# Kernel optimization log

Hardware: AMD Instinct MI355X
Metric: run time of the kernel (lower is better)

## Reference

```python
import jax, jax.numpy as jnp
import numpy as np

FEAT_STRIDE = 32  # 520 // 16
POOL = 7          # adaptive_avg_pool2d target (7,7)
C = 8             # channels consumed as (2 classes x 4 coords)


def setup_inputs() -> dict:
    key = jax.random.key(0)
    k1, k2, k3 = jax.random.split(key, 3)
    H = W = 1024
    conv_out = jax.random.normal(k1, (1, C, H, W), dtype=jnp.float32)
    n = 8192
    # sample pixel-space coords in [0, H*FEAT_STRIDE) and sort so min<=max per axis
    ys = jnp.sort(jax.random.randint(k2, (n, 2), 0, H * FEAT_STRIDE), axis=1)
    xs = jnp.sort(jax.random.randint(k3, (n, 2), 0, W * FEAT_STRIDE), axis=1)
    rois = jnp.stack([ys[:, 0], xs[:, 0], ys[:, 1], xs[:, 1]], axis=1).astype(jnp.int64)
    return {"conv_out": conv_out, "rois": rois}


def _adaptive_bounds(start, length):
    # PyTorch adaptive_avg_pool2d bin edges over [start, start+length)
    j = jnp.arange(POOL)
    lo = start + (j * length) // POOL
    hi = start + ((j + 1) * length + POOL - 1) // POOL  # ceil div
    return lo, hi


def _forward(conv_out, rois):
    r = rois // FEAT_STRIDE
    x = conv_out[0]  # [C, H, W]
    # summed-area table, padded so sat[:, y, x] = sum over [0:y, 0:x)
    sat = jnp.pad(jnp.cumsum(jnp.cumsum(x, axis=1), axis=2),
                  ((0, 0), (1, 0), (1, 0)))  # [C, H+1, W+1]

    def pool_one(roi):
        ymin, xmin = roi[0], roi[1]
        ymax, xmax = roi[2] + 1, roi[3] + 1  # exclusive ends
        ylo, yhi = _adaptive_bounds(ymin, ymax - ymin)
        xlo, xhi = _adaptive_bounds(xmin, xmax - xmin)
        # 7x7 bin sums via inclusion-exclusion on SAT -> [C,7,7]
        s = (sat[:, yhi[:, None], xhi[None, :]]
             - sat[:, ylo[:, None], xhi[None, :]]
             - sat[:, yhi[:, None], xlo[None, :]]
             + sat[:, ylo[:, None], xlo[None, :]])
        area = ((yhi - ylo)[:, None] * (xhi - xlo)[None, :]).astype(s.dtype)
        block7 = s / area                       # adaptive_avg_pool2d -> (7,7)
        return block7.mean(axis=(1, 2))         # adaptive_avg_pool2d -> (1,1), [C]

    pooled = jax.vmap(pool_one)(r)              # [n, C]
    return pooled.reshape(-1, 2, 4)


def reference(conv_out, rois):
    return _forward(conv_out, rois)
```

## Files before the change

kernel.cpp:

```cpp
#include <hip/hip_runtime.h>
#include <cstddef>
#include <cstdint>

#define SATW 1025
#define W8   8200
#define NCH  8

__global__ __launch_bounds__(256) void rowscan_kernel(const float* __restrict__ in,
                                                      float* __restrict__ sat) {
    const int y    = blockIdx.x;
    const int t    = threadIdx.x;
    const int lane = t & 63;
    const int wv   = t >> 6;

    __shared__ float lds[NCH][1024];

    for (int k = 0; k < 2; ++k) {
        const int c = wv * 2 + k;
        const float4* r4 = (const float4*)(in + ((size_t)c * 1024 + y) * 1024);
        double chunkbase = 0.0;
#pragma unroll
        for (int j = 0; j < 4; ++j) {
            float4 a = r4[lane + 64 * j];
            double v0 = a.x, v1 = a.y, v2 = a.z, v3 = a.w;
            double s = v0 + v1 + v2 + v3;
            double ps = s;
#pragma unroll
            for (int off = 1; off < 64; off <<= 1) {
                double n = __shfl_up(ps, off, 64);
                if (lane >= off) ps += n;
            }
            double base = chunkbase + ps - s;
            double p0 = base + v0, p1 = p0 + v1, p2 = p1 + v2, p3 = p2 + v3;
            float4 o = make_float4((float)p0, (float)p1, (float)p2, (float)p3);
            ((float4*)lds[c])[lane + 64 * j] = o;
            chunkbase += __shfl(ps, 63, 64);
        }
    }
    __syncthreads();

    float* orow = sat + (size_t)(y + 1) * W8;
    for (int f4 = t; f4 < W8 / 4; f4 += 256) {
        int f = f4 * 4;
        float4 o;
        float* po = (float*)&o;
#pragma unroll
        for (int j = 0; j < 4; ++j) {
            int ff = f + j;
            int x = ff >> 3, c = ff & 7;
            po[j] = x ? lds[c][x - 1] : 0.0f;
        }
        ((float4*)orow)[f4] = o;
    }
}

__global__ void colsum_kernel(const float* __restrict__ sat,
                              double* __restrict__ partial, int R) {
    int f  = blockIdx.x * 256 + threadIdx.x;
    int ch = blockIdx.y;
    if (f >= W8) return;
    const float* p = sat + ((size_t)(1 + ch * R)) * W8 + f;
    double s = 0.0;
#pragma unroll 4
    for (int i = 0; i < R; ++i) s += (double)p[(size_t)i * W8];
    partial[(size_t)ch * W8 + f] = s;
}

__global__ void scanpartial_kernel(double* __restrict__ partial, int C) {
    int f = blockIdx.x * 256 + threadIdx.x;
    if (f >= W8) return;
    double run = 0.0;
    for (int ch = 0; ch < C; ++ch) {
        double v = partial[(size_t)ch * W8 + f];
        partial[(size_t)ch * W8 + f] = run;
        run += v;
    }
}

__global__ void colscan_kernel(float* __restrict__ sat,
                               const double* __restrict__ partial, int R) {
    int f  = blockIdx.x * 256 + threadIdx.x;
    int ch = blockIdx.y;
    if (f >= W8) return;
    double run = partial[(size_t)ch * W8 + f];
    if (ch == 0) sat[f] = 0.0f;
    float* p = sat + ((size_t)(1 + ch * R)) * W8 + f;
#pragma unroll 4
    for (int i = 0; i < R; ++i) {
        run += (double)p[(size_t)i * W8];
        p[(size_t)i * W8] = (float)run;
    }
}

__global__ __launch_bounds__(256) void pool_kernel(const float* __restrict__ sat,
                                                   const int* __restrict__ rois,
                                                   float* __restrict__ out,
                                                   int n_roi) {
    int lane = threadIdx.x & 63;
    int roi  = (blockIdx.x * blockDim.x + threadIdx.x) >> 6;
    if (roi >= n_roi) return;

    const int4 rv = ((const int4*)rois)[roi];
    int ymin = rv.x >> 5;
    int xmin = rv.y >> 5;
    int Ly   = (rv.z >> 5) + 1 - ymin;
    int Lx   = (rv.w >> 5) + 1 - xmin;

    double acc[NCH];
#pragma unroll
    for (int c = 0; c < NCH; ++c) acc[c] = 0.0;

    if (lane < 49) {
        int by = lane / 7;
        int bx = lane - by * 7;
        int ylo = ymin + (by * Ly) / 7;
        int yhi = ymin + ((by + 1) * Ly + 6) / 7;
        int xlo = xmin + (bx * Lx) / 7;
        int xhi = xmin + ((bx + 1) * Lx + 6) / 7;
        double inv = 1.0 / (double)((yhi - ylo) * (xhi - xlo));

        const float4* hh = (const float4*)(sat + ((size_t)yhi * SATW + xhi) * NCH);
        const float4* lh = (const float4*)(sat + ((size_t)ylo * SATW + xhi) * NCH);
        const float4* hl = (const float4*)(sat + ((size_t)yhi * SATW + xlo) * NCH);
        const float4* ll = (const float4*)(sat + ((size_t)ylo * SATW + xlo) * NCH);
        float4 a0 = hh[0], a1 = hh[1];
        float4 b0 = lh[0], b1 = lh[1];
        float4 c0 = hl[0], c1 = hl[1];
        float4 d0 = ll[0], d1 = ll[1];
        const float* pa = (const float*)&a0;
        const float* pb = (const float*)&b0;
        const float* pc = (const float*)&c0;
        const float* pd = (const float*)&d0;
        float4 tmpa[2] = {a0, a1}, tmpb[2] = {b0, b1}, tmpc[2] = {c0, c1}, tmpd[2] = {d0, d1};
        const float* fa = (const float*)tmpa;
        const float* fb = (const float*)tmpb;
        const float* fc = (const float*)tmpc;
        const float* fd = (const float*)tmpd;
        (void)pa; (void)pb; (void)pc; (void)pd;
#pragma unroll
        for (int c = 0; c < NCH; ++c) {
            double v = (double)fa[c] - (double)fb[c] - (double)fc[c] + (double)fd[c];
            acc[c] = v * inv;
        }
    }

#pragma unroll
    for (int off = 32; off; off >>= 1) {
#pragma unroll
        for (int c = 0; c < NCH; ++c) acc[c] += __shfl_down(acc[c], off, 64);
    }

    if (lane == 0) {
        float4 o0 = make_float4((float)(acc[0] * (1.0 / 49.0)),
                                (float)(acc[1] * (1.0 / 49.0)),
                                (float)(acc[2] * (1.0 / 49.0)),
                                (float)(acc[3] * (1.0 / 49.0)));
        float4 o1 = make_float4((float)(acc[4] * (1.0 / 49.0)),
                                (float)(acc[5] * (1.0 / 49.0)),
                                (float)(acc[6] * (1.0 / 49.0)),
                                (float)(acc[7] * (1.0 / 49.0)));
        float4* po = (float4*)(out + (size_t)roi * NCH);
        po[0] = o0;
        po[1] = o1;
    }
}

extern "C" void kernel_launch(void* const* d_in, const int* in_sizes, int n_in,
                              void* d_out, int out_size, void* d_ws, size_t ws_size,
                              hipStream_t stream) {
    const float* conv = (const float*)d_in[0];
    const int*   rois = (const int*)d_in[1];
    float*       out  = (float*)d_out;
    int n_roi = in_sizes[1] / 4;

    const size_t sat_bytes = (size_t)SATW * W8 * 4;
    int C = 64;
    while (C > 8 && sat_bytes + (size_t)C * W8 * 8 > ws_size) C >>= 1;
    int R = 1024 / C;

    float*  sat     = (float*)d_ws;
    double* partial = (double*)((char*)d_ws + sat_bytes);

    rowscan_kernel<<<1024, 256, 0, stream>>>(conv, sat);
    colsum_kernel<<<dim3(33, C), 256, 0, stream>>>(sat, partial, R);
    scanpartial_kernel<<<33, 256, 0, stream>>>(partial, C);
    colscan_kernel<<<dim3(33, C), 256, 0, stream>>>(sat, partial, R);
    pool_kernel<<<(n_roi + 3) / 4, 256, 0, stream>>>(sat, rois, out, n_roi);
}
```

Before: 134.7 us.

## Replace three-pass column scan with single-pass decoupled look-back chained scan

The colsum, scanpartial and colscan kernels are replaced by one chained kernel. Each block takes a 16-row chunk of a 1024-wide column slice through a ticket counter, keeps the chunk in registers, publishes its aggregate, and looks back over earlier chunks' flags to get its prefix before writing the scanned rows. This removes one full read pass over the SAT and two kernel launches, in exchange for spin-waiting on flags and atomics. The control flags are zeroed inside the row-scan kernel.

```diff
diff --git a/kernel.cpp b/kernel.cpp
--- a/kernel.cpp
+++ b/kernel.cpp
@@ -5,13 +5,29 @@
 #define SATW 1025
 #define W8   8200
 #define NCH  8
+#define ROWS 16
+#define NCHUNK 64
+#define NSLICE 9
+#define SLICEW 1024
+
+#define SAT_BYTES ((size_t)SATW * W8 * 4)
+#define CTRL_OFF  ((SAT_BYTES + 255) & ~(size_t)255)
+#define CTRL_INTS (16 + NSLICE * NCHUNK)
+#define AGG_OFF   (CTRL_OFF + 4096)
+#define AGG_BYTES ((size_t)NSLICE * NCHUNK * SLICEW * 8)
+#define INCL_OFF  (AGG_OFF + AGG_BYTES)
 
 __global__ __launch_bounds__(256) void rowscan_kernel(const float* __restrict__ in,
-                                                      float* __restrict__ sat) {
+                                                      float* __restrict__ sat,
+                                                      int* __restrict__ ctrl) {
     const int y    = blockIdx.x;
     const int t    = threadIdx.x;
     const int lane = t & 63;
     const int wv   = t >> 6;
+
+    if (y == 0) {
+        for (int i = t; i < CTRL_INTS; i += 256) ctrl[i] = 0;
+    }
 
     __shared__ float lds[NCH][1024];
 
@@ -32,8 +48,8 @@
             }
             double base = chunkbase + ps - s;
             double p0 = base + v0, p1 = p0 + v1, p2 = p1 + v2, p3 = p2 + v3;
-            float4 o = make_float4((float)p0, (float)p1, (float)p2, (float)p3);
-            ((float4*)lds[c])[lane + 64 * j] = o;
+            ((float4*)lds[c])[lane + 64 * j] =
+                make_float4((float)p0, (float)p1, (float)p2, (float)p3);
             chunkbase += __shfl(ps, 63, 64);
         }
     }
@@ -54,41 +70,94 @@
     }
 }
 
-__global__ void colsum_kernel(const float* __restrict__ sat,
-                              double* __restrict__ partial, int R) {
-    int f  = blockIdx.x * 256 + threadIdx.x;
-    int ch = blockIdx.y;
-    if (f >= W8) return;
-    const float* p = sat + ((size_t)(1 + ch * R)) * W8 + f;
-    double s = 0.0;
-#pragma unroll 4
-    for (int i = 0; i < R; ++i) s += (double)p[(size_t)i * W8];
-    partial[(size_t)ch * W8 + f] = s;
-}
-
-__global__ void scanpartial_kernel(double* __restrict__ partial, int C) {
-    int f = blockIdx.x * 256 + threadIdx.x;
-    if (f >= W8) return;
-    double run = 0.0;
-    for (int ch = 0; ch < C; ++ch) {
-        double v = partial[(size_t)ch * W8 + f];
-        partial[(size_t)ch * W8 + f] = run;
-        run += v;
-    }
-}
-
-__global__ void colscan_kernel(float* __restrict__ sat,
-                               const double* __restrict__ partial, int R) {
-    int f  = blockIdx.x * 256 + threadIdx.x;
-    int ch = blockIdx.y;
-    if (f >= W8) return;
-    double run = partial[(size_t)ch * W8 + f];
-    if (ch == 0) sat[f] = 0.0f;
-    float* p = sat + ((size_t)(1 + ch * R)) * W8 + f;
-#pragma unroll 4
-    for (int i = 0; i < R; ++i) {
-        run += (double)p[(size_t)i * W8];
-        p[(size_t)i * W8] = (float)run;
+__global__ __launch_bounds__(256) void colscan_chained(float* __restrict__ sat,
+                                                       double* __restrict__ agg,
+                                                       double* __restrict__ incl,
+                                                       int* __restrict__ ctrl) {
+    const int slice = blockIdx.x;
+    const int t     = threadIdx.x;
+    int* tickets = ctrl;
+    int* flags   = ctrl + 16;
+
+    __shared__ int sh_chunk;
+    if (t == 0) sh_chunk = atomicAdd(&tickets[slice], 1);
+    __syncthreads();
+    const int chunk = sh_chunk;
+
+    const int  col = slice * SLICEW + t * 4;
+    const bool act = col < W8;
+
+    float4 r[ROWS];
+    double s0 = 0, s1 = 0, s2 = 0, s3 = 0;
+    float* base = sat + (size_t)(1 + chunk * ROWS) * W8 + col;
+    if (act) {
+#pragma unroll
+        for (int i = 0; i < ROWS; ++i) {
+            r[i] = *(const float4*)(base + (size_t)i * W8);
+            s0 += r[i].x; s1 += r[i].y; s2 += r[i].z; s3 += r[i].w;
+        }
+    }
+
+    const size_t vo  = ((size_t)slice * NCHUNK + chunk) * SLICEW + (size_t)t * 4;
+    int*         flg = &flags[slice * NCHUNK + chunk];
+    double e0 = 0, e1 = 0, e2 = 0, e3 = 0;
+
+    if (chunk == 0) {
+        __hip_atomic_store(&incl[vo + 0], s0, __ATOMIC_RELAXED, __HIP_MEMORY_SCOPE_AGENT);
+        __hip_atomic_store(&incl[vo + 1], s1, __ATOMIC_RELAXED, __HIP_MEMORY_SCOPE_AGENT);
+        __hip_atomic_store(&incl[vo + 2], s2, __ATOMIC_RELAXED, __HIP_MEMORY_SCOPE_AGENT);
+        __hip_atomic_store(&incl[vo + 3], s3, __ATOMIC_RELAXED, __HIP_MEMORY_SCOPE_AGENT);
+        __threadfence();
+        __syncthreads();
+        if (t == 0) __hip_atomic_store(flg, 2, __ATOMIC_RELEASE, __HIP_MEMORY_SCOPE_AGENT);
+    } else {
+        __hip_atomic_store(&agg[vo + 0], s0, __ATOMIC_RELAXED, __HIP_MEMORY_SCOPE_AGENT);
+        __hip_atomic_store(&agg[vo + 1], s1, __ATOMIC_RELAXED, __HIP_MEMORY_SCOPE_AGENT);
+        __hip_atomic_store(&agg[vo + 2], s2, __ATOMIC_RELAXED, __HIP_MEMORY_SCOPE_AGENT);
+        __hip_atomic_store(&agg[vo + 3], s3, __ATOMIC_RELAXED, __HIP_MEMORY_SCOPE_AGENT);
+        __threadfence();
+        __syncthreads();
+        if (t == 0) __hip_atomic_store(flg, 1, __ATOMIC_RELEASE, __HIP_MEMORY_SCOPE_AGENT);
+
+        __shared__ int sh_st;
+        for (int p = chunk - 1; ; --p) {
+            if (t == 0) {
+                int st;
+                do {
+                    st = __hip_atomic_load(&flags[slice * NCHUNK + p],
+                                           __ATOMIC_ACQUIRE, __HIP_MEMORY_SCOPE_AGENT);
+                } while (st == 0);
+                sh_st = st;
+            }
+            __syncthreads();
+            const int st = sh_st;
+            __syncthreads();
+            const double* src = (st == 2 ? incl : agg) +
+                                ((size_t)slice * NCHUNK + p) * SLICEW + (size_t)t * 4;
+            e0 += __hip_atomic_load(&src[0], __ATOMIC_RELAXED, __HIP_MEMORY_SCOPE_AGENT);
+            e1 += __hip_atomic_load(&src[1], __ATOMIC_RELAXED, __HIP_MEMORY_SCOPE_AGENT);
+            e2 += __hip_atomic_load(&src[2], __ATOMIC_RELAXED, __HIP_MEMORY_SCOPE_AGENT);
+            e3 += __hip_atomic_load(&src[3], __ATOMIC_RELAXED, __HIP_MEMORY_SCOPE_AGENT);
+            if (st == 2) break;
+        }
+        __hip_atomic_store(&incl[vo + 0], e0 + s0, __ATOMIC_RELAXED, __HIP_MEMORY_SCOPE_AGENT);
+        __hip_atomic_store(&incl[vo + 1], e1 + s1, __ATOMIC_RELAXED, __HIP_MEMORY_SCOPE_AGENT);
+        __hip_atomic_store(&incl[vo + 2], e2 + s2, __ATOMIC_RELAXED, __HIP_MEMORY_SCOPE_AGENT);
+        __hip_atomic_store(&incl[vo + 3], e3 + s3, __ATOMIC_RELAXED, __HIP_MEMORY_SCOPE_AGENT);
+        __threadfence();
+        __syncthreads();
+        if (t == 0) __hip_atomic_store(flg, 2, __ATOMIC_RELEASE, __HIP_MEMORY_SCOPE_AGENT);
+    }
+
+    if (act) {
+        if (chunk == 0) *(float4*)(sat + col) = make_float4(0.f, 0.f, 0.f, 0.f);
+        double r0 = e0, r1 = e1, r2 = e2, r3 = e3;
+#pragma unroll
+        for (int i = 0; i < ROWS; ++i) {
+            r0 += r[i].x; r1 += r[i].y; r2 += r[i].z; r3 += r[i].w;
+            *(float4*)(base + (size_t)i * W8) =
+                make_float4((float)r0, (float)r1, (float)r2, (float)r3);
+        }
     }
 }
 
@@ -119,24 +188,19 @@
         int xhi = xmin + ((bx + 1) * Lx + 6) / 7;
         double inv = 1.0 / (double)((yhi - ylo) * (xhi - xlo));
 
+        float4 a[2], b[2], c4[2], d[2];
         const float4* hh = (const float4*)(sat + ((size_t)yhi * SATW + xhi) * NCH);
         const float4* lh = (const float4*)(sat + ((size_t)ylo * SATW + xhi) * NCH);
         const float4* hl = (const float4*)(sat + ((size_t)yhi * SATW + xlo) * NCH);
         const float4* ll = (const float4*)(sat + ((size_t)ylo * SATW + xlo) * NCH);
-        float4 a0 = hh[0], a1 = hh[1];
-        float4 b0 = lh[0], b1 = lh[1];
-        float4 c0 = hl[0], c1 = hl[1];
-        float4 d0 = ll[0], d1 = ll[1];
-        const float* pa = (const float*)&a0;
-        const float* pb = (const float*)&b0;
-        const float* pc = (const float*)&c0;
-        const float* pd = (const float*)&d0;
-        float4 tmpa[2] = {a0, a1}, tmpb[2] = {b0, b1}, tmpc[2] = {c0, c1}, tmpd[2] = {d0, d1};
-        const float* fa = (const float*)tmpa;
-        const float* fb = (const float*)tmpb;
-        const float* fc = (const float*)tmpc;
-        const float* fd = (const float*)tmpd;
-        (void)pa; (void)pb; (void)pc; (void)pd;
+        a[0] = hh[0]; a[1] = hh[1];
+        b[0] = lh[0]; b[1] = lh[1];
+        c4[0] = hl[0]; c4[1] = hl[1];
+        d[0] = ll[0]; d[1] = ll[1];
+        const float* fa = (const float*)a;
+        const float* fb = (const float*)b;
+        const float* fc = (const float*)c4;
+        const float* fd = (const float*)d;
 #pragma unroll
         for (int c = 0; c < NCH; ++c) {
             double v = (double)fa[c] - (double)fb[c] - (double)fc[c] + (double)fd[c];
@@ -151,17 +215,15 @@
     }
 
     if (lane == 0) {
-        float4 o0 = make_float4((float)(acc[0] * (1.0 / 49.0)),
-                                (float)(acc[1] * (1.0 / 49.0)),
-                                (float)(acc[2] * (1.0 / 49.0)),
-                                (float)(acc[3] * (1.0 / 49.0)));
-        float4 o1 = make_float4((float)(acc[4] * (1.0 / 49.0)),
-                                (float)(acc[5] * (1.0 / 49.0)),
-                                (float)(acc[6] * (1.0 / 49.0)),
-                                (float)(acc[7] * (1.0 / 49.0)));
         float4* po = (float4*)(out + (size_t)roi * NCH);
-        po[0] = o0;
-        po[1] = o1;
+        po[0] = make_float4((float)(acc[0] * (1.0 / 49.0)),
+                            (float)(acc[1] * (1.0 / 49.0)),
+                            (float)(acc[2] * (1.0 / 49.0)),
+                            (float)(acc[3] * (1.0 / 49.0)));
+        po[1] = make_float4((float)(acc[4] * (1.0 / 49.0)),
+                            (float)(acc[5] * (1.0 / 49.0)),
+                            (float)(acc[6] * (1.0 / 49.0)),
+                            (float)(acc[7] * (1.0 / 49.0)));
     }
 }
 
@@ -173,17 +235,12 @@
     float*       out  = (float*)d_out;
     int n_roi = in_sizes[1] / 4;
 
-    const size_t sat_bytes = (size_t)SATW * W8 * 4;
-    int C = 64;
-    while (C > 8 && sat_bytes + (size_t)C * W8 * 8 > ws_size) C >>= 1;
-    int R = 1024 / C;
-
-    float*  sat     = (float*)d_ws;
-    double* partial = (double*)((char*)d_ws + sat_bytes);
-
-    rowscan_kernel<<<1024, 256, 0, stream>>>(conv, sat);
-    colsum_kernel<<<dim3(33, C), 256, 0, stream>>>(sat, partial, R);
-    scanpartial_kernel<<<33, 256, 0, stream>>>(partial, C);
-    colscan_kernel<<<dim3(33, C), 256, 0, stream>>>(sat, partial, R);
+    float*  sat  = (float*)d_ws;
+    int*    ctrl = (int*)((char*)d_ws + CTRL_OFF);
+    double* agg  = (double*)((char*)d_ws + AGG_OFF);
+    double* incl = (double*)((char*)d_ws + INCL_OFF);
+
+    rowscan_kernel<<<1024, 256, 0, stream>>>(conv, sat, ctrl);
+    colscan_chained<<<dim3(NSLICE, NCHUNK), 256, 0, stream>>>(sat, agg, incl, ctrl);
     pool_kernel<<<(n_roi + 3) / 4, 256, 0, stream>>>(sat, rois, out, n_roi);
 }
```

Result: slower. 336.5 us (+149.7%).
